# Kernel optimization log

Measured on AMD Instinct MI355X. Metric: run time of the kernel, lower is better.

## Reference

```python
import jax, jax.numpy as jnp
import numpy as np

B, S, C, H = 8, 1024, 512, 8
DH = C // H  # channels per head


def setup_inputs() -> dict:
    key = jax.random.key(0)
    ks = jax.random.split(key, 10)
    s = 1.0 / np.sqrt(C)
    return {
        "pe_lin_encoding": jax.random.normal(ks[0], (B, S, C), jnp.float32),
        "pe_lin_skip": jax.random.normal(ks[1], (B, S, C), jnp.float32),
        "Wq": jax.random.normal(ks[2], (C, C), jnp.float32) * s,
        "bq": jax.random.normal(ks[3], (C,), jnp.float32) * s,
        "Wk": jax.random.normal(ks[4], (C, C), jnp.float32) * s,
        "bk": jax.random.normal(ks[5], (C,), jnp.float32) * s,
        "Wv": jax.random.normal(ks[6], (C, C), jnp.float32) * s,
        "bv": jax.random.normal(ks[7], (C,), jnp.float32) * s,
        "Wo": jax.random.normal(ks[8], (C, C), jnp.float32) * s,
        "bo": jax.random.normal(ks[9], (C,), jnp.float32) * s,
    }


def reference(pe_lin_encoding, pe_lin_skip, Wq, bq, Wk, bk, Wv, bv, Wo, bo):
    # flatten trailing dims (already [B, S, C] here)
    x = pe_lin_encoding.reshape(pe_lin_encoding.shape[0], pe_lin_encoding.shape[1], -1)
    # torch Linear convention: y = x @ W^T + b, W is [out, in]
    q = jnp.einsum("bsc,oc->bso", x, Wq) + bq
    k = jnp.einsum("bsc,oc->bso", x, Wk) + bk
    v = jnp.einsum("bsc,oc->bso", x, Wv) + bv
    # split heads: [B, S, H, DH] -> attention per head
    q = q.reshape(B, S, H, DH)
    k = k.reshape(B, S, H, DH)
    v = v.reshape(B, S, H, DH)
    scale = 1.0 / np.sqrt(DH)
    scores = jnp.einsum("bqhd,bkhd->bhqk", q, k) * scale  # [B,H,S,S]
    attn = jax.nn.softmax(scores, axis=-1)
    ctx = jnp.einsum("bhqk,bkhd->bqhd", attn, v).reshape(B, S, C)
    out = jnp.einsum("bsc,oc->bso", ctx, Wo) + bo
    return out + pe_lin_skip
```

## Files before the change

kernel.cpp:

```cpp
#include <hip/hip_runtime.h>
#include <hip/hip_bf16.h>

typedef unsigned short u16;
typedef unsigned int u32;

constexpr int B  = 8;
constexpr int S  = 1024;
constexpr int C  = 512;
constexpr int H  = 8;
constexpr int DH = 64;
constexpr int M  = B * S;

typedef __attribute__((ext_vector_type(8))) short bf16x8;
typedef __attribute__((ext_vector_type(4))) float f32x4;
typedef __attribute__((ext_vector_type(16))) float f32x16;
typedef __attribute__((ext_vector_type(4))) u32 u32x4;

#define GLOBAL_AS __attribute__((address_space(1)))
#define LDS_AS    __attribute__((address_space(3)))

#define QSCALE 0.1803368867f

__device__ __forceinline__ float bf2f(u16 u) {
    return __uint_as_float(((u32)u) << 16);
}
__device__ __forceinline__ u16 f2bf(float f) {
    u32 u = __float_as_uint(f);
    u += 0x7fffu + ((u >> 16) & 1u);
    return (u16)(u >> 16);
}
__device__ __forceinline__ u32 pack2(float a, float b) {
    return (u32)f2bf(a) | ((u32)f2bf(b) << 16);
}
__device__ __forceinline__ u32 cvtpk(float a, float b) {
    u32 d;
    asm("v_cvt_pk_bf16_f32 %0, %1, %2" : "=v"(d) : "v"(a), "v"(b));
    return d;
}
__device__ __forceinline__ void async_cp16(const u16* g, u16* l) {
    __builtin_amdgcn_global_load_lds((const GLOBAL_AS void*)g, (LDS_AS void*)l, 16, 0, 0);
}
__device__ __forceinline__ f32x16 zero16() {
    f32x16 z;
    #pragma unroll
    for (int i = 0; i < 16; i++) z[i] = 0.f;
    return z;
}

constexpr int NX4 = M * C / 4;
constexpr int NW4 = C * C / 4;

__global__ __launch_bounds__(256) void cvt_kernel(
    const float* __restrict__ x,
    const float* __restrict__ wq, const float* __restrict__ wk,
    const float* __restrict__ wv, const float* __restrict__ wo,
    u16* __restrict__ xb, u16* __restrict__ wqkv, u16* __restrict__ wob)
{
    const int i = blockIdx.x * 256 + threadIdx.x;
    const float* src; u16* dst; int off;
    if      (i < NX4)          { src = x;  dst = xb;           off = i; }
    else if (i < NX4 +   NW4)  { src = wq; dst = wqkv;         off = i - NX4; }
    else if (i < NX4 + 2*NW4)  { src = wk; dst = wqkv + C*C;   off = i - NX4 -   NW4; }
    else if (i < NX4 + 3*NW4)  { src = wv; dst = wqkv + 2*C*C; off = i - NX4 - 2*NW4; }
    else                       { src = wo; dst = wob;          off = i - NX4 - 3*NW4; }
    float4 v = ((const float4*)src)[off];
    uint2 p; p.x = pack2(v.x, v.y); p.y = pack2(v.z, v.w);
    ((uint2*)dst)[off] = p;
}

__global__ __launch_bounds__(256) void qkv_gemm(
    const u16* __restrict__ xb, const u16* __restrict__ wqkv,
    const float* __restrict__ bq, const float* __restrict__ bk,
    const float* __restrict__ bv,
    u16* __restrict__ Qo, u16* __restrict__ Ko, u16* __restrict__ Vo)
{
    __shared__ alignas(16) u16 smem[128 * 96];
    u16* const Asm = smem;
    u16* const Bsm = smem + 128 * 64;

    const int mTile = blockIdx.x * 128;
    const int nTile = blockIdx.y * 64;
    const int t = threadIdx.x, lane = t & 63, w = t >> 6;
    const int ql = lane & 15, quad = lane >> 4;
    const int wm = (w & 1) * 64, wn = (w >> 1) * 32;

    f32x4 acc[4][2];
    #pragma unroll
    for (int i = 0; i < 4; i++)
        #pragma unroll
        for (int j = 0; j < 2; j++) acc[i][j] = (f32x4){0.f, 0.f, 0.f, 0.f};

    for (int k0 = 0; k0 < C; k0 += 64) {
        __syncthreads();
        #pragma unroll
        for (int q = 0; q < 4; q++) {
            const int chunk = q * 256 + t;
            const int row = chunk >> 3, c8 = (chunk & 7) * 8;
            async_cp16(xb + (size_t)(mTile + row) * C + k0 + c8, &Asm[row * 64 + c8]);
        }
        #pragma unroll
        for (int q = 0; q < 2; q++) {
            const int chunk = q * 256 + t;
            const int row = chunk >> 3, c8 = (chunk & 7) * 8;
            async_cp16(wqkv + (size_t)(nTile + row) * C + k0 + c8, &Bsm[row * 64 + c8]);
        }
        __syncthreads();

        #pragma unroll
        for (int ks = 0; ks < 64; ks += 32) {
            bf16x8 af[4], bfr[2];
            #pragma unroll
            for (int i = 0; i < 4; i++)
                af[i] = *(const bf16x8*)&Asm[(wm + i*16 + ql) * 64 + ks + quad*8];
            #pragma unroll
            for (int j = 0; j < 2; j++)
                bfr[j] = *(const bf16x8*)&Bsm[(wn + j*16 + ql) * 64 + ks + quad*8];
            #pragma unroll
            for (int i = 0; i < 4; i++)
                #pragma unroll
                for (int j = 0; j < 2; j++)
                    acc[i][j] = __builtin_amdgcn_mfma_f32_16x16x32_bf16(af[i], bfr[j], acc[i][j], 0, 0, 0);
        }
    }

    const int z = nTile >> 9;
    const int nBase = nTile & 511;
    const int bb = mTile >> 10, ssBase = mTile & 1023;
    if (z == 2) {
        __syncthreads();
        u16* const T = smem;
        #pragma unroll
        for (int j = 0; j < 2; j++) {
            const int n = wn + j*16 + ql;
            const float bj = bv[nBase + n];
            #pragma unroll
            for (int i = 0; i < 4; i++)
                #pragma unroll
                for (int r = 0; r < 4; r++)
                    T[n * 136 + wm + i*16 + quad*4 + r] = f2bf(acc[i][j][r] + bj);
        }
        __syncthreads();
        #pragma unroll
        for (int q = 0; q < 4; q++) {
            const int c = q * 256 + t;
            const int row = c >> 4, col = (c & 15) * 8;
            const int o = nBase + row, h = o >> 6, d = o & 63;
            *(float4*)(Vo + ((size_t)((bb*H + h) * DH + d)) * S + ssBase + col) =
                *(const float4*)&T[row * 136 + col];
        }
    } else {
        const float* bias = (z == 0) ? bq : bk;
        u16* dst          = (z == 0) ? Qo : Ko;
        const float sc    = (z == 0) ? QSCALE : 1.0f;
        const int h = nBase >> 6;
        __syncthreads();
        u16* const T = smem;
        #pragma unroll
        for (int j = 0; j < 2; j++) {
            const int n = wn + j*16 + ql;
            const float bj = bias[nBase + n];
            #pragma unroll
            for (int i = 0; i < 4; i++)
                #pragma unroll
                for (int r = 0; r < 4; r++)
                    T[(wm + i*16 + quad*4 + r) * 72 + n] = f2bf((acc[i][j][r] + bj) * sc);
        }
        __syncthreads();
        #pragma unroll
        for (int q = 0; q < 4; q++) {
            const int c = q * 256 + t;
            const int row = c >> 3, col = (c & 7) * 8;
            *(float4*)(dst + ((size_t)((bb*H + h) * S + (ssBase + row))) * DH + col) =
                *(const float4*)&T[row * 72 + col];
        }
    }
}

__global__ __launch_bounds__(256) void attn_kernel(
    const u16* __restrict__ Qo,
    const u16* __restrict__ Ko,
    const u16* __restrict__ Vo,
    u16* __restrict__ ctx)
{
    __shared__ alignas(16) u16 KVs[2][2][2][64 * 64];

    const int g = blockIdx.x;
    const int xcd = g & 7, slot = g >> 3;
    const int bh = xcd * 8 + (slot >> 4);
    const int qt = slot & 15;

    const int t = threadIdx.x;
    const int lane = t & 63, w = t >> 6;
    const int qg = w & 1, kg = w >> 1;
    const int l31 = lane & 31, hi = lane >> 5;
    const int sxh8 = ((l31 & 7) ^ hi) << 3;
    const int kRow = l31 * 64;

    const u16* __restrict__ Qb = Qo + (size_t)bh * S * DH;
    const u16* __restrict__ Kb = Ko + (size_t)bh * S * DH;
    const u16* __restrict__ Vt = Vo + (size_t)bh * DH * S;

    const int qrow = qt * 64 + qg * 32 + l31;
    bf16x8 qf[4];
    #pragma unroll
    for (int ks = 0; ks < 4; ks++)
        qf[ks] = *(const bf16x8*)(Qb + (size_t)qrow * DH + ks * 16 + hi * 8);

    bf16x8 onesf;
    #pragma unroll
    for (int i = 0; i < 8; i++) onesf[i] = (short)0x3F80;

    f32x16 acc[2], accl;
    acc[0] = zero16(); acc[1] = zero16(); accl = zero16();

    const int tp = t & 127;
    const int kBase = kg * 512;

    auto STAGE = [&](int buf, int it) {
        const int k0 = kBase + it * 64;
        u16* const Kd = &KVs[buf][kg][0][0];
        u16* const Vd = &KVs[buf][kg][1][0];
        #pragma unroll
        for (int q = 0; q < 4; ++q) {
            const int gi = q * 128 + tp;
            const int row = gi >> 3, cc = gi & 7;
            const int c = cc ^ (row & 7);
            async_cp16(Kb + (size_t)(k0 + row) * DH + c * 8, &Kd[gi * 8]);
            async_cp16(Vt + (size_t)row * S + k0 + c * 8,    &Vd[gi * 8]);
        }
    };

    STAGE(0, 0);
    #pragma unroll 2
    for (int it = 0; it < 8; ++it) {
        const int cur = it & 1;
        if (it + 1 < 8) {
            STAGE(cur ^ 1, it + 1);
            asm volatile("s_waitcnt vmcnt(8)" ::: "memory");
        } else {
            asm volatile("s_waitcnt vmcnt(0)" ::: "memory");
        }
        asm volatile("s_barrier" ::: "memory");

        const u16* const Kh = &KVs[cur][kg][0][0];
        const u16* const Vh = &KVs[cur][kg][1][0];

        #pragma unroll
        for (int kt = 0; kt < 2; ++kt) {
            f32x16 sc = zero16();
            #pragma unroll
            for (int ks = 0; ks < 4; ++ks) {
                const bf16x8 kf = *(const bf16x8*)&Kh[kRow + kt * 2048 + ((ks << 4) ^ sxh8)];
                sc = __builtin_amdgcn_mfma_f32_32x32x16_bf16(kf, qf[ks], sc, 0, 0, 0);
            }
            #pragma unroll
            for (int s = 0; s < 2; ++s) {
                float e0 = exp2f(sc[8*s+0]), e1 = exp2f(sc[8*s+1]);
                float e2 = exp2f(sc[8*s+2]), e3 = exp2f(sc[8*s+3]);
                float e4 = exp2f(sc[8*s+4]), e5 = exp2f(sc[8*s+5]);
                float e6 = exp2f(sc[8*s+6]), e7 = exp2f(sc[8*s+7]);
                u32 x0 = cvtpk(e0, e1), x1 = cvtpk(e2, e3);
                u32 y0 = cvtpk(e4, e5), y1 = cvtpk(e6, e7);
                asm("v_permlane32_swap_b32 %0, %1" : "+v"(x0), "+v"(y0));
                asm("v_permlane32_swap_b32 %0, %1" : "+v"(x1), "+v"(y1));
                u32x4 pw; pw.x = x0; pw.y = x1; pw.z = y0; pw.w = y1;
                const bf16x8 pa = __builtin_bit_cast(bf16x8, pw);

                const int ccol = (((kt * 4 + s * 2) << 3) ^ sxh8);
                acc[0] = __builtin_amdgcn_mfma_f32_32x32x16_bf16(
                    pa, *(const bf16x8*)&Vh[kRow + ccol], acc[0], 0, 0, 0);
                acc[1] = __builtin_amdgcn_mfma_f32_32x32x16_bf16(
                    pa, *(const bf16x8*)&Vh[kRow + 2048 + ccol], acc[1], 0, 0, 0);
                accl = __builtin_amdgcn_mfma_f32_32x32x16_bf16(pa, onesf, accl, 0, 0, 0);
            }
        }
        asm volatile("s_barrier" ::: "memory");
    }

    __syncthreads();
    float* F = (float*)&KVs[0][0][0][0];
    if (kg == 1) {
        #pragma unroll
        for (int r = 0; r < 16; ++r) F[r * 128 + qg * 64 + lane] = acc[0][r];
        #pragma unroll
        for (int r = 0; r < 16; ++r) F[(16 + r) * 128 + qg * 64 + lane] = acc[1][r];
        #pragma unroll
        for (int r = 0; r < 16; ++r) F[(32 + r) * 128 + qg * 64 + lane] = accl[r];
    }
    __syncthreads();
    if (kg == 0) {
        #pragma unroll
        for (int r = 0; r < 16; ++r) acc[0][r] += F[r * 128 + qg * 64 + lane];
        #pragma unroll
        for (int r = 0; r < 16; ++r) acc[1][r] += F[(16 + r) * 128 + qg * 64 + lane];
        #pragma unroll
        for (int r = 0; r < 16; ++r) accl[r]   += F[(32 + r) * 128 + qg * 64 + lane];

        const int b_ = bh >> 3, h = bh & 7;
        const int qbase2 = qt * 64 + qg * 32 + 4 * hi;
        #pragma unroll
        for (int r = 0; r < 16; ++r) {
            const float inv = 1.0f / accl[r];
            const int srow = qbase2 + (r & 3) + 8 * (r >> 2);
            const size_t base = ((size_t)(b_ * S + srow)) * C + h * DH + l31;
            ctx[base]      = f2bf(acc[0][r] * inv);
            ctx[base + 32] = f2bf(acc[1][r] * inv);
        }
    }
}

__global__ __launch_bounds__(256) void out_gemm(
    const u16* __restrict__ ctx, const u16* __restrict__ wob,
    const float* __restrict__ bo, const float* __restrict__ skip,
    float* __restrict__ out)
{
    __shared__ alignas(16) u16 smem[8704];
    u16* const Asm = smem;
    u16* const Bsm = smem + 64 * 64;

    const int mTile = blockIdx.x * 64;
    const int nTile = blockIdx.y * 64;
    const int t = threadIdx.x, lane = t & 63, w = t >> 6;
    const int ql = lane & 15, quad = lane >> 4;
    const int wm = (w & 1) * 32, wn = (w >> 1) * 32;

    f32x4 acc[2][2];
    #pragma unroll
    for (int i = 0; i < 2; i++)
        #pragma unroll
        for (int j = 0; j < 2; j++) acc[i][j] = (f32x4){0.f, 0.f, 0.f, 0.f};

    for (int k0 = 0; k0 < C; k0 += 64) {
        __syncthreads();
        #pragma unroll
        for (int q = 0; q < 2; q++) {
            const int chunk = q * 256 + t;
            const int row = chunk >> 3, c8 = (chunk & 7) * 8;
            async_cp16(ctx + (size_t)(mTile + row) * C + k0 + c8, &Asm[row * 64 + c8]);
        }
        #pragma unroll
        for (int q = 0; q < 2; q++) {
            const int chunk = q * 256 + t;
            const int row = chunk >> 3, c8 = (chunk & 7) * 8;
            async_cp16(wob + (size_t)(nTile + row) * C + k0 + c8, &Bsm[row * 64 + c8]);
        }
        __syncthreads();

        #pragma unroll
        for (int ks = 0; ks < 64; ks += 32) {
            bf16x8 af[2], bfr[2];
            #pragma unroll
            for (int i = 0; i < 2; i++)
                af[i] = *(const bf16x8*)&Asm[(wm + i*16 + ql) * 64 + ks + quad*8];
            #pragma unroll
            for (int j = 0; j < 2; j++)
                bfr[j] = *(const bf16x8*)&Bsm[(wn + j*16 + ql) * 64 + ks + quad*8];
            #pragma unroll
            for (int i = 0; i < 2; i++)
                #pragma unroll
                for (int j = 0; j < 2; j++)
                    acc[i][j] = __builtin_amdgcn_mfma_f32_16x16x32_bf16(af[i], bfr[j], acc[i][j], 0, 0, 0);
        }
    }

    float* const F2 = (float*)smem;
    __syncthreads();
    #pragma unroll
    for (int j = 0; j < 2; j++) {
        const int n = wn + j*16 + ql;
        #pragma unroll
        for (int i = 0; i < 2; i++)
            #pragma unroll
            for (int r = 0; r < 4; r++)
                F2[(wm + i*16 + quad*4 + r) * 68 + n] = acc[i][j][r];
    }
    __syncthreads();
    #pragma unroll
    for (int q8 = 0; q8 < 4; ++q8) {
        const int c = q8 * 256 + t;
        const int row = c >> 4, col4 = (c & 15) * 4;
        const int m = mTile + row, o = nTile + col4;
        const float4 v  = *(const float4*)&F2[row * 68 + col4];
        const float4 s4 = *(const float4*)&skip[(size_t)m * C + o];
        const float4 b4 = *(const float4*)&bo[o];
        float4 r4;
        r4.x = v.x + b4.x + s4.x;  r4.y = v.y + b4.y + s4.y;
        r4.z = v.z + b4.z + s4.z;  r4.w = v.w + b4.w + s4.w;
        *(float4*)&out[(size_t)m * C + o] = r4;
    }
}

extern "C" void kernel_launch(void* const* d_in, const int* in_sizes, int n_in,
                              void* d_out, int out_size, void* d_ws, size_t ws_size,
                              hipStream_t stream) {
    (void)in_sizes; (void)n_in; (void)out_size; (void)ws_size;
    const float* x    = (const float*)d_in[0];
    const float* skip = (const float*)d_in[1];
    const float* Wq   = (const float*)d_in[2];
    const float* bq   = (const float*)d_in[3];
    const float* Wk   = (const float*)d_in[4];
    const float* bk   = (const float*)d_in[5];
    const float* Wv   = (const float*)d_in[6];
    const float* bv   = (const float*)d_in[7];
    const float* Wo   = (const float*)d_in[8];
    const float* bo   = (const float*)d_in[9];
    float* out = (float*)d_out;

    u16* xb   = (u16*)d_ws;
    u16* wqkv = xb   + (size_t)M * C;
    u16* wob  = wqkv + (size_t)3 * C * C;
    u16* Qo   = wob  + (size_t)C * C;
    u16* Ko   = Qo   + (size_t)B * H * S * DH;
    u16* Vo   = Ko   + (size_t)B * H * S * DH;
    u16* ctx  = xb;

    cvt_kernel<<<dim3((NX4 + 4 * NW4) / 256), 256, 0, stream>>>(
        x, Wq, Wk, Wv, Wo, xb, wqkv, wob);
    qkv_gemm<<<dim3(M / 128, 1536 / 64), 256, 0, stream>>>(
        xb, wqkv, bq, bk, bv, Qo, Ko, Vo);
    attn_kernel<<<dim3(1024), 256, 0, stream>>>(Qo, Ko, Vo, ctx);
    out_gemm<<<dim3(M / 64, C / 64), 256, 0, stream>>>(
        ctx, wob, bo, skip, out);
}
```

Baseline: 171.6 us.

## Single-buffer attention K/V staging and prefetch skip tensor in output GEMM

The attention kernel drops its double-buffered async K/V staging and goes to one LDS buffer with __syncthreads around each load. Per-thread source pointers are precomputed and advanced each iteration. This halves the kernel's static shared memory, likely to fit more blocks per CU, but it gives up the overlap of the next tile's loads with the current tile's MFMA work. Separately, the output GEMM issues its skip-tensor and bias loads before the K loop, so their latency is hidden behind the matmul, at the cost of extra registers.

```diff
diff --git a/kernel.cpp b/kernel.cpp
--- a/kernel.cpp
+++ b/kernel.cpp
@@ -182,7 +182,7 @@
     const u16* __restrict__ Vo,
     u16* __restrict__ ctx)
 {
-    __shared__ alignas(16) u16 KVs[2][2][2][64 * 64];
+    __shared__ alignas(16) u16 KVs[2][2][64 * 64];
 
     const int g = blockIdx.x;
     const int xcd = g & 7, slot = g >> 3;
@@ -216,34 +216,32 @@
     const int tp = t & 127;
     const int kBase = kg * 512;
 
-    auto STAGE = [&](int buf, int it) {
-        const int k0 = kBase + it * 64;
-        u16* const Kd = &KVs[buf][kg][0][0];
-        u16* const Vd = &KVs[buf][kg][1][0];
+    const u16* kPtr[4]; const u16* vPtr[4];
+    u16* kDst[4]; u16* vDst[4];
+    #pragma unroll
+    for (int q = 0; q < 4; ++q) {
+        const int gi = q * 128 + tp;
+        const int row = gi >> 3, cc = gi & 7;
+        const int c = cc ^ (row & 7);
+        kPtr[q] = Kb + (size_t)(kBase + row) * DH + c * 8;
+        vPtr[q] = Vt + (size_t)row * S + kBase + c * 8;
+        kDst[q] = &KVs[kg][0][gi * 8];
+        vDst[q] = &KVs[kg][1][gi * 8];
+    }
+
+    for (int it = 0; it < 8; ++it) {
+        __syncthreads();
         #pragma unroll
         for (int q = 0; q < 4; ++q) {
-            const int gi = q * 128 + tp;
-            const int row = gi >> 3, cc = gi & 7;
-            const int c = cc ^ (row & 7);
-            async_cp16(Kb + (size_t)(k0 + row) * DH + c * 8, &Kd[gi * 8]);
-            async_cp16(Vt + (size_t)row * S + k0 + c * 8,    &Vd[gi * 8]);
-        }
-    };
-
-    STAGE(0, 0);
-    #pragma unroll 2
-    for (int it = 0; it < 8; ++it) {
-        const int cur = it & 1;
-        if (it + 1 < 8) {
-            STAGE(cur ^ 1, it + 1);
-            asm volatile("s_waitcnt vmcnt(8)" ::: "memory");
-        } else {
-            asm volatile("s_waitcnt vmcnt(0)" ::: "memory");
-        }
-        asm volatile("s_barrier" ::: "memory");
-
-        const u16* const Kh = &KVs[cur][kg][0][0];
-        const u16* const Vh = &KVs[cur][kg][1][0];
+            async_cp16(kPtr[q], kDst[q]);
+            async_cp16(vPtr[q], vDst[q]);
+            kPtr[q] += 64 * DH;
+            vPtr[q] += 64;
+        }
+        __syncthreads();
+
+        const u16* const Kh = &KVs[kg][0][0];
+        const u16* const Vh = &KVs[kg][1][0];
 
         #pragma unroll
         for (int kt = 0; kt < 2; ++kt) {
@@ -274,11 +272,10 @@
                 accl = __builtin_amdgcn_mfma_f32_32x32x16_bf16(pa, onesf, accl, 0, 0, 0);
             }
         }
-        asm volatile("s_barrier" ::: "memory");
     }
 
     __syncthreads();
-    float* F = (float*)&KVs[0][0][0][0];
+    float* F = (float*)&KVs[0][0][0];
     if (kg == 1) {
         #pragma unroll
         for (int r = 0; r < 16; ++r) F[r * 128 + qg * 64 + lane] = acc[0][r];
@@ -324,6 +321,13 @@
     const int ql = lane & 15, quad = lane >> 4;
     const int wm = (w & 1) * 32, wn = (w >> 1) * 32;
 
+    const int erow = t >> 4, ecol = (t & 15) * 4;
+    float4 sk[4];
+    #pragma unroll
+    for (int q8 = 0; q8 < 4; ++q8)
+        sk[q8] = *(const float4*)&skip[(size_t)(mTile + q8*16 + erow) * C + nTile + ecol];
+    const float4 b4 = *(const float4*)&bo[nTile + ecol];
+
     f32x4 acc[2][2];
     #pragma unroll
     for (int i = 0; i < 2; i++)
@@ -377,16 +381,12 @@
     __syncthreads();
     #pragma unroll
     for (int q8 = 0; q8 < 4; ++q8) {
-        const int c = q8 * 256 + t;
-        const int row = c >> 4, col4 = (c & 15) * 4;
-        const int m = mTile + row, o = nTile + col4;
-        const float4 v  = *(const float4*)&F2[row * 68 + col4];
-        const float4 s4 = *(const float4*)&skip[(size_t)m * C + o];
-        const float4 b4 = *(const float4*)&bo[o];
+        const int row = q8*16 + erow;
+        const float4 v = *(const float4*)&F2[row * 68 + ecol];
         float4 r4;
-        r4.x = v.x + b4.x + s4.x;  r4.y = v.y + b4.y + s4.y;
-        r4.z = v.z + b4.z + s4.z;  r4.w = v.w + b4.w + s4.w;
-        *(float4*)&out[(size_t)m * C + o] = r4;
+        r4.x = v.x + b4.x + sk[q8].x;  r4.y = v.y + b4.y + sk[q8].y;
+        r4.z = v.z + b4.z + sk[q8].z;  r4.w = v.w + b4.w + sk[q8].w;
+        *(float4*)&out[(size_t)(mTile + row) * C + nTile + ecol] = r4;
     }
 }
 
```

Result: no change. 171.8 us (+0.1%).
